# Kernel optimization log

Measured on AMD Instinct MI355X. Metric: run time of the kernel, lower is better.

The kernel has to match this reference:

```python
import jax, jax.numpy as jnp
import numpy as np

B, N, D, H, FF, L = 4, 256, 240, 8, 1024, 4
HD = D // H  # 30, divisible by 3 for 3D rotary
EPS = 1e-5


def setup_inputs() -> dict:
    key = jax.random.key(0)
    ks = iter(jax.random.split(key, 40))
    def nrm(shape, scale=1.0):
        return jax.random.normal(next(ks), shape, jnp.float32) * scale
    inp = {}
    for n in ["hand_token_t", "head_token_t", "hand_token_m1", "head_token_m1"]:
        inp[n] = nrm((B, N, D))
    for n in ["coords_hand_t", "coords_head_t", "coords_hand_m1", "coords_head_m1"]:
        inp[n] = jax.random.uniform(next(ks), (B, N, 3), jnp.float32)
    for n in ["state_t", "state_m1", "hand_pose_m1", "head_pose_m1", "hand_pose_t", "head_pose_t"]:
        inp[n] = nrm((B, D))
    sd = float(np.sqrt(2.0 / D))   # kaiming_normal fan_in=D
    sf = float(np.sqrt(2.0 / FF))  # kaiming_normal fan_in=FF
    inp["Wq"] = nrm((L, D, D), sd); inp["Wk"] = nrm((L, D, D), sd)
    inp["Wv"] = nrm((L, D, D), sd); inp["Wo"] = nrm((L, D, D), sd)
    inp["W1"] = nrm((L, FF, D), sd); inp["W2"] = nrm((L, D, FF), sf)
    inp["bq"] = jnp.zeros((L, D)); inp["bk"] = jnp.zeros((L, D))
    inp["bv"] = jnp.zeros((L, D)); inp["bo"] = jnp.zeros((L, D))
    inp["b1"] = jnp.zeros((L, FF)); inp["b2"] = jnp.zeros((L, D))
    inp["g1"] = jnp.ones((L, D)); inp["be1"] = jnp.zeros((L, D))
    inp["g2"] = jnp.ones((L, D)); inp["be2"] = jnp.zeros((L, D))
    return inp


def rope3d(x, coords):
    # x: (B,H,S,HD); coords: (B,S,3). head_dim split into 3 axis blocks,
    # each block rotated (interleaved pairs) by RoPE with pos = coord along that axis.
    d = HD // 3
    inv = 1.0 / (10000.0 ** (jnp.arange(0, d, 2, dtype=jnp.float32) / d))  # (d//2,)
    outs = []
    for a in range(3):
        xa = x[..., a * d:(a + 1) * d]
        ang = coords[:, None, :, a, None] * inv  # (B,1,S,d//2)
        c, s = jnp.cos(ang), jnp.sin(ang)
        x1, x2 = xa[..., 0::2], xa[..., 1::2]
        outs.append(jnp.stack([x1 * c - x2 * s, x1 * s + x2 * c], -1).reshape(xa.shape))
    if HD % 3:
        outs.append(x[..., 3 * d:])
    return jnp.concatenate(outs, -1)


def layernorm(x, g, b):
    m = x.mean(-1, keepdims=True)
    v = jnp.mean((x - m) ** 2, -1, keepdims=True)
    return (x - m) * jax.lax.rsqrt(v + EPS) * g + b


def _forward(hand_token_t, head_token_t, hand_token_m1, head_token_m1,
             coords_hand_t, coords_head_t, coords_hand_m1, coords_head_m1,
             state_t, state_m1, hand_pose_m1, head_pose_m1, hand_pose_t, head_pose_t,
             Wq, bq, Wk, bk, Wv, bv, Wo, bo, W1, b1, W2, b2, g1, be1, g2, be2):
    z3 = jnp.zeros((B, 1, 3), jnp.float32)
    src = jnp.concatenate([
        state_m1[:, None], hand_pose_m1[:, None], head_pose_m1[:, None],
        hand_token_m1, head_token_m1,
        state_t[:, None], hand_pose_t[:, None], head_pose_t[:, None],
        hand_token_t, head_token_t], axis=1)            # (B, S, D)
    cs = jnp.concatenate([z3, z3, z3, coords_hand_m1, coords_head_m1,
                          z3, z3, z3, coords_hand_t, coords_head_t], axis=1)  # (B, S, 3)
    S = src.shape[1]
    past = 1 + 2 + 2 * N  # current-frame tokens hide the past-frame keys
    mask = jnp.zeros((S, S), bool).at[past:, :past].set(True)
    scale = 1.0 / float(np.sqrt(HD))
    for l in range(L):
        q = (src @ Wq[l].T + bq[l]).reshape(B, S, H, HD).transpose(0, 2, 1, 3)
        k = (src @ Wk[l].T + bk[l]).reshape(B, S, H, HD).transpose(0, 2, 1, 3)
        v = (src @ Wv[l].T + bv[l]).reshape(B, S, H, HD).transpose(0, 2, 1, 3)
        q = rope3d(q, cs)
        k = rope3d(k, cs)
        scores = jnp.einsum('bhqd,bhkd->bhqk', q, k) * scale
        scores = jnp.where(mask, -jnp.inf, scores)
        attn = jnp.einsum('bhqk,bhkd->bhqd', jax.nn.softmax(scores, axis=-1), v)
        attn = attn.transpose(0, 2, 1, 3).reshape(B, S, D)
        s2 = layernorm(src + attn @ Wo[l].T + bo[l], g1[l], be1[l])
        ff = jax.nn.gelu(s2 @ W1[l].T + b1[l], approximate=False) @ W2[l].T + b2[l]
        src = layernorm(s2 + ff, g2[l], be2[l])
    return src[:, past:, :]


def reference(hand_token_t, head_token_t, hand_token_m1, head_token_m1,
              coords_hand_t, coords_head_t, coords_hand_m1, coords_head_m1,
              state_t, state_m1, hand_pose_m1, head_pose_m1, hand_pose_t, head_pose_t,
              Wq, bq, Wk, bk, Wv, bv, Wo, bo, W1, b1, W2, b2, g1, be1, g2, be2):
    return _forward(hand_token_t, head_token_t, hand_token_m1, head_token_m1,
                    coords_hand_t, coords_head_t, coords_hand_m1, coords_head_m1,
                    state_t, state_m1, hand_pose_m1, head_pose_m1, hand_pose_t, head_pose_t,
                    Wq, bq, Wk, bk, Wv, bv, Wo, bo, W1, b1, W2, b2, g1, be1, g2, be2)
```

## Files before the change

kernel.cpp:

```cpp
#include <hip/hip_runtime.h>
#include <cmath>

constexpr int cB = 4, cN = 256, cD = 240, cH = 8, cFF = 1024, cL = 4;
constexpr int cHD = 30;
constexpr int cS2 = 515;
constexpr int cBS2 = cB * cS2;
constexpr int cKp = 256;
constexpr int cSP2 = 576;
constexpr float EPSF = 1e-5f;

typedef __bf16 bf16x8 __attribute__((ext_vector_type(8)));
typedef float f32x4 __attribute__((ext_vector_type(4)));

__device__ inline unsigned short f2bf(float f) {
    unsigned int u = __builtin_bit_cast(unsigned int, f);
    unsigned int r = (u + 0x7fffu + ((u >> 16) & 1u)) >> 16;
    return (unsigned short)r;
}

constexpr int R1 = 4 * cL * 65536;
constexpr int R2 = R1 + cL * 1024 * 256;
constexpr int R3 = R2 + cL * 256 * 1024;
constexpr int R4 = R3 + cBS2 * cD;
constexpr int R5 = R4 + cBS2 * 15;
constexpr size_t qkvN = (size_t)cB * cH * cSP2 * 32;
constexpr int nSpan32 = (int)(3 * qkvN / 2);
constexpr int R6 = R5 + nSpan32;
constexpr int R7 = R6 + cBS2 * 8;

__global__ __launch_bounds__(256) void setup_all(
    const float* __restrict__ Wq, const float* __restrict__ Wk,
    const float* __restrict__ Wv, const float* __restrict__ Wo,
    const float* __restrict__ W1, const float* __restrict__ W2,
    const float* __restrict__ hand_t, const float* __restrict__ head_t,
    const float* __restrict__ state_t,
    const float* __restrict__ hand_pose_t, const float* __restrict__ head_pose_t,
    const float* __restrict__ ch_t, const float* __restrict__ cd_t,
    unsigned short* __restrict__ wqkv, unsigned short* __restrict__ w1p,
    unsigned short* __restrict__ w2p,
    float* __restrict__ src, unsigned short* __restrict__ sbf,
    float2* __restrict__ trig,
    unsigned int* __restrict__ qkvspan,
    unsigned short* __restrict__ padA, unsigned short* __restrict__ padB,
    unsigned short* __restrict__ padC)
{
    int idx = blockIdx.x * 256 + threadIdx.x;
    if (idx < R1) {
        int which = idx >> 18;
        const float* W = (which == 0) ? Wq : (which == 1) ? Wk : (which == 2) ? Wv : Wo;
        int rem = idx & 262143;
        int m = rem >> 16;
        int rc = rem & 65535;
        int r = rc >> 8, c = rc & 255;
        float v = (r < 240 && c < 240) ? W[((size_t)m * 240 + r) * 240 + c] : 0.f;
        wqkv[idx] = f2bf(v);
    } else if (idx < R2) {
        int rem = idx - R1;
        int m = rem >> 18;
        int rc = rem & 262143;
        int r = rc >> 8, c = rc & 255;
        float v = (c < 240) ? W1[((size_t)m * 1024 + r) * 240 + c] : 0.f;
        w1p[rem] = f2bf(v);
    } else if (idx < R3) {
        int rem = idx - R2;
        int m = rem >> 18;
        int rc = rem & 262143;
        int r = rc >> 10, c = rc & 1023;
        float v = (r < 240) ? W2[((size_t)m * 240 + r) * 1024 + c] : 0.f;
        w2p[rem] = f2bf(v);
    } else if (idx < R4) {
        int rem = idx - R3;
        int d = rem % cD;
        int r = rem / cD;
        int b = r / cS2, s = r % cS2;
        const float* p; int off;
        if (s == 0)          { p = state_t;      off = b * cD + d; }
        else if (s == 1)     { p = hand_pose_t;  off = b * cD + d; }
        else if (s == 2)     { p = head_pose_t;  off = b * cD + d; }
        else if (s < 259)    { p = hand_t;       off = (b * cN + (s - 3)) * cD + d; }
        else                 { p = head_t;       off = (b * cN + (s - 259)) * cD + d; }
        float v = p[off];
        src[rem] = v;
        sbf[(size_t)r * cKp + d] = f2bf(v);
    } else if (idx < R5) {
        int rem = idx - R4;
        int r = rem / 15, pair = rem - r * 15;
        int b = r / cS2, s = r % cS2;
        int a = pair / 5, j = pair - a * 5;
        float coord = 0.f;
        if (s >= 3 && s < 259)       coord = ch_t[(b * cN + (s - 3)) * 3 + a];
        else if (s >= 259)           coord = cd_t[(b * cN + (s - 259)) * 3 + a];
        float inv = __expf(-1.8420680743952367f * (float)j);
        float sn, co;
        sincosf(coord * inv, &sn, &co);
        trig[rem] = make_float2(co, sn);
    } else if (idx < R6) {
        qkvspan[idx - R5] = 0u;
    } else if (idx < R7) {
        int rem = idx - R6;
        int r = rem >> 3, j = rem & 7;
        ((unsigned int*)(padA + (size_t)r * 256 + 240))[j] = 0u;
        ((unsigned int*)(padB + (size_t)r * 256 + 240))[j] = 0u;
        ((unsigned int*)(padC + (size_t)r * 256 + 240))[j] = 0u;
    }
}

#define GEMM_CORE64(A_PTR, W_PTR, M_, KA_, NK_)                                               \
    __shared__ unsigned short Al[64][72];                                                     \
    __shared__ unsigned short Bl[64][72];                                                     \
    const int tid = threadIdx.x;                                                              \
    const int lane = tid & 63;                                                                \
    const int w = tid >> 6;                                                                   \
    const int wm = w >> 1, wn = w & 1;                                                        \
    const int lrow = lane & 15, kq = lane >> 4;                                               \
    const int colBase = blockIdx.x * 64;                                                      \
    const int sRow = tid >> 2;                                                                \
    const int sC = (tid & 3) * 16;                                                            \
    const int ar0 = min(rowBase + sRow, M_ - 1);                                              \
    const int wr = colBase + sRow;                                                            \
    const unsigned short* a0p = A_PTR + (size_t)ar0 * KA_ + sC;                               \
    const unsigned short* wp  = W_PTR + (size_t)wr * KA_ + sC;                                \
    f32x4 acc[2][2] = {};                                                                     \
    int4 rA0a = *(const int4*)a0p, rA0b = *(const int4*)(a0p + 8);                            \
    int4 rBa  = *(const int4*)wp,  rBb  = *(const int4*)(wp + 8);                             \
    for (int ks = 0; ks < NK_; ++ks) {                                                        \
        __syncthreads();                                                                      \
        *(int4*)&Al[sRow][sC]     = rA0a;                                                     \
        *(int4*)&Al[sRow][sC + 8] = rA0b;                                                     \
        *(int4*)&Bl[sRow][sC]     = rBa;                                                      \
        *(int4*)&Bl[sRow][sC + 8] = rBb;                                                      \
        __syncthreads();                                                                      \
        if (ks + 1 < NK_) {                                                                   \
            int kk = (ks + 1) * 64;                                                           \
            rA0a = *(const int4*)(a0p + kk); rA0b = *(const int4*)(a0p + kk + 8);             \
            rBa  = *(const int4*)(wp + kk);  rBb  = *(const int4*)(wp + kk + 8);              \
        }                                                                                     \
        _Pragma("unroll")                                                                     \
        for (int sub = 0; sub < 2; ++sub) {                                                   \
            bf16x8 af[2], bfr[2];                                                             \
            _Pragma("unroll")                                                                 \
            for (int i = 0; i < 2; ++i)                                                       \
                af[i] = *(const bf16x8*)&Al[wm * 32 + i * 16 + lrow][sub * 32 + kq * 8];      \
            _Pragma("unroll")                                                                 \
            for (int j = 0; j < 2; ++j)                                                       \
                bfr[j] = *(const bf16x8*)&Bl[wn * 32 + j * 16 + lrow][sub * 32 + kq * 8];     \
            _Pragma("unroll")                                                                 \
            for (int i = 0; i < 2; ++i)                                                       \
                _Pragma("unroll")                                                             \
                for (int j = 0; j < 2; ++j)                                                   \
                    acc[i][j] = __builtin_amdgcn_mfma_f32_16x16x32_bf16(af[i], bfr[j], acc[i][j], 0, 0, 0); \
        }                                                                                     \
    }

__global__ __launch_bounds__(256) void gemm_qkv_rope(
    const unsigned short* __restrict__ A,
    const unsigned short* __restrict__ Wqp, const unsigned short* __restrict__ Wkp,
    const unsigned short* __restrict__ Wvp,
    const float* __restrict__ bq, const float* __restrict__ bk, const float* __restrict__ bv,
    const float2* __restrict__ trig,
    unsigned short* __restrict__ qbf, unsigned short* __restrict__ kbf,
    unsigned short* __restrict__ vtbf)
{
    const int z = blockIdx.z;
    const unsigned short* Wsel = (z == 0) ? Wqp : (z == 1) ? Wkp : Wvp;
    const float* bias = (z == 0) ? bq : (z == 1) ? bk : bv;
    const int rowBase = blockIdx.y * 64;
    GEMM_CORE64(A, Wsel, cBS2, cKp, 4)
    if (z == 2) {
#pragma unroll
        for (int i = 0; i < 2; ++i) {
#pragma unroll
            for (int j = 0; j < 2; ++j) {
                int col = colBase + wn * 32 + j * 16 + lrow;
                if (col >= cD) continue;
                float bcol = bias[col];
                int hh = col / cHD, hd = col % cHD;
                f32x4 vv = acc[i][j];
                int row0 = rowBase + wm * 32 + i * 16 + kq * 4;
                int b0 = row0 / cS2, s0 = row0 - b0 * cS2;
                if (row0 + 3 < cBS2 && s0 + 3 < cS2) {
                    unsigned int lo = (unsigned)f2bf(vv[0] + bcol) | ((unsigned)f2bf(vv[1] + bcol) << 16);
                    unsigned int hi = (unsigned)f2bf(vv[2] + bcol) | ((unsigned)f2bf(vv[3] + bcol) << 16);
                    size_t base = ((size_t)(b0 * cH + hh) * 32 + hd) * cSP2 + s0;
                    *(unsigned int*)&vtbf[base]     = lo;
                    *(unsigned int*)&vtbf[base + 2] = hi;
                } else {
#pragma unroll
                    for (int r = 0; r < 4; ++r) {
                        int row = row0 + r;
                        if (row >= cBS2) continue;
                        int bb = row / cS2, ss = row - bb * cS2;
                        vtbf[((size_t)(bb * cH + hh) * 32 + hd) * cSP2 + ss] = f2bf(vv[r] + bcol);
                    }
                }
            }
        }
    } else {
        unsigned short* dst = (z == 0) ? qbf : kbf;
#pragma unroll
        for (int i = 0; i < 2; ++i) {
#pragma unroll
            for (int j = 0; j < 2; ++j) {
                int col = colBase + wn * 32 + j * 16 + lrow;
                bool colok = col < cD;
                int cc = colok ? col : 0;
                float bcol = colok ? bias[cc] : 0.f;
                int hh = cc / cHD, hd = cc % cHD;
                int a3 = hd / 10, jj = (hd % 10) >> 1;
                int pair = a3 * 5 + jj;
                f32x4 vv = acc[i][j];
#pragma unroll
                for (int r = 0; r < 2 * 2; ++r) {
                    int row = rowBase + wm * 32 + i * 16 + kq * 4 + r;
                    bool rowok = row < cBS2;
                    int rowc = rowok ? row : 0;
                    float val = vv[r] + bcol;
                    float pval = __shfl_xor(val, 1);
                    float2 t = trig[rowc * 15 + pair];
                    float outv = (hd & 1) ? (pval * t.y + val * t.x) : (val * t.x - pval * t.y);
                    if (colok && rowok) {
                        int b = rowc / cS2, s = rowc - b * cS2;
                        dst[((size_t)(b * cH + hh) * cSP2 + s) * 32 + hd] = f2bf(outv);
                    }
                }
            }
        }
    }
}

__global__ __launch_bounds__(256) void attn_mfma(
    const unsigned short* __restrict__ qbf, const unsigned short* __restrict__ kbf,
    const unsigned short* __restrict__ vtbf, unsigned short* __restrict__ outb)
{
    __shared__ unsigned short Pl[4][16][72];
    __shared__ float Ol[4][16][33];
    __shared__ float Ml[4][16];
    __shared__ float Ll[4][16];
    const int tid = threadIdx.x, lane = tid & 63, w = tid >> 6;
    const int bh = blockIdx.y, b = bh >> 3, h = bh & 7;
    const int qbase = blockIdx.x * 16;
    const int lr = lane & 15, lg = lane >> 4;
    const float scl = 0.18257418583505536f;
    const f32x4 czero = {0.f, 0.f, 0.f, 0.f};
    bf16x8 qf = *(const bf16x8*)&qbf[((size_t)bh * cSP2 + qbase + lr) * 32 + lg * 8];
    float m[4], l[4];
    f32x4 o0 = czero, o1 = czero;
#pragma unroll
    for (int r = 0; r < 4; ++r) { m[r] = -3.0e38f; l[r] = 0.f; }
    const int ts = (w * 9) / 4;
    const int te = ((w + 1) * 9) / 4;
    for (int tt = ts; tt < te; ++tt) {
        const int kb = tt * 64;
        f32x4 c[4];
#pragma unroll
        for (int t = 0; t < 4; ++t) {
            bf16x8 kf = *(const bf16x8*)&kbf[((size_t)bh * cSP2 + kb + 16 * t + lr) * 32 + lg * 8];
            c[t] = __builtin_amdgcn_mfma_f32_16x16x32_bf16(qf, kf, czero, 0, 0, 0);
        }
#pragma unroll
        for (int t = 0; t < 4; ++t) {
            bool koob = (kb + 16 * t + lr) >= cS2;
#pragma unroll
            for (int r = 0; r < 4; ++r)
                c[t][r] = koob ? -3.0e38f : c[t][r] * scl;
        }
        float mx[4];
#pragma unroll
        for (int r = 0; r < 4; ++r)
            mx[r] = fmaxf(fmaxf(c[0][r], c[1][r]), fmaxf(c[2][r], c[3][r]));
#pragma unroll
        for (int off = 1; off < 16; off <<= 1)
#pragma unroll
            for (int r = 0; r < 4; ++r)
                mx[r] = fmaxf(mx[r], __shfl_xor(mx[r], off));
        float corr[4], me[4], ps[4];
#pragma unroll
        for (int r = 0; r < 4; ++r) {
            float mn = fmaxf(m[r], mx[r]);
            corr[r] = __expf(m[r] - mn);
            m[r] = mn;
            me[r] = fmaxf(mn, -1.0e30f);
            ps[r] = 0.f;
        }
#pragma unroll
        for (int t = 0; t < 4; ++t)
#pragma unroll
            for (int r = 0; r < 4; ++r) {
                float p = __expf(c[t][r] - me[r]);
                c[t][r] = p;
                ps[r] += p;
            }
#pragma unroll
        for (int off = 1; off < 16; off <<= 1)
#pragma unroll
            for (int r = 0; r < 4; ++r)
                ps[r] += __shfl_xor(ps[r], off);
#pragma unroll
        for (int r = 0; r < 4; ++r) {
            l[r] = l[r] * corr[r] + ps[r];
            o0[r] *= corr[r];
            o1[r] *= corr[r];
        }
#pragma unroll
        for (int t = 0; t < 4; ++t)
#pragma unroll
            for (int r = 0; r < 4; ++r)
                Pl[w][lg * 4 + r][16 * t + lr] = f2bf(c[t][r]);
#pragma unroll
        for (int c2 = 0; c2 < 2; ++c2) {
            bf16x8 pa  = *(const bf16x8*)&Pl[w][lr][c2 * 32 + lg * 8];
            bf16x8 bv0 = *(const bf16x8*)&vtbf[((size_t)bh * 32 + lr) * cSP2 + kb + c2 * 32 + lg * 8];
            bf16x8 bv1 = *(const bf16x8*)&vtbf[((size_t)bh * 32 + 16 + lr) * cSP2 + kb + c2 * 32 + lg * 8];
            o0 = __builtin_amdgcn_mfma_f32_16x16x32_bf16(pa, bv0, o0, 0, 0, 0);
            o1 = __builtin_amdgcn_mfma_f32_16x16x32_bf16(pa, bv1, o1, 0, 0, 0);
        }
    }
#pragma unroll
    for (int r = 0; r < 4; ++r) {
        int row = lg * 4 + r;
        if (lr == 0) { Ml[w][row] = m[r]; Ll[w][row] = l[r]; }
        Ol[w][row][lr]      = o0[r];
        Ol[w][row][16 + lr] = o1[r];
    }
    __syncthreads();
    if (w == 0) {
        const int col = lane & 31, half = lane >> 5;
#pragma unroll
        for (int rr = 0; rr < 8; ++rr) {
            int row = half * 8 + rr;
            float M = fmaxf(fmaxf(Ml[0][row], Ml[1][row]), fmaxf(Ml[2][row], Ml[3][row]));
            float Lt = 0.f, Ot = 0.f;
#pragma unroll
            for (int ww = 0; ww < 4; ++ww) {
                float cc = __expf(Ml[ww][row] - M);
                Lt += Ll[ww][row] * cc;
                Ot += Ol[ww][row][col] * cc;
            }
            int qq = qbase + row;
            if (qq < cS2 && col < cHD)
                outb[((size_t)(b * cS2 + qq)) * cKp + h * cHD + col] = f2bf(Ot / Lt);
        }
    }
}

__global__ __launch_bounds__(256) void gemm_res64(
    const unsigned short* __restrict__ A, const unsigned short* __restrict__ W,
    const float* __restrict__ bias, const float* __restrict__ Rs,
    float* __restrict__ outF)
{
    const int rowBase = blockIdx.y * 64;
    GEMM_CORE64(A, W, cBS2, cKp, 4)
#pragma unroll
    for (int i = 0; i < 2; ++i) {
#pragma unroll
        for (int j = 0; j < 2; ++j) {
            int col = colBase + wn * 32 + j * 16 + lrow;
            if (col >= cD) continue;
            float bcol = bias[col];
            f32x4 v = acc[i][j];
#pragma unroll
            for (int r = 0; r < 4; ++r) {
                int row = rowBase + wm * 32 + i * 16 + kq * 4 + r;
                if (row >= cBS2) continue;
                outF[(size_t)row * cD + col] = v[r] + bcol + Rs[(size_t)row * cD + col];
            }
        }
    }
}

__global__ __launch_bounds__(256) void gemm_ff1(
    const unsigned short* __restrict__ A, const unsigned short* __restrict__ W,
    const float* __restrict__ bias, unsigned short* __restrict__ outB)
{
    const int rowBase = blockIdx.y * 64;
    GEMM_CORE64(A, W, cBS2, cKp, 4)
#pragma unroll
    for (int i = 0; i < 2; ++i) {
#pragma unroll
        for (int j = 0; j < 2; ++j) {
            int col = colBase + wn * 32 + j * 16 + lrow;
            float bcol = bias[col];
            f32x4 v = acc[i][j];
#pragma unroll
            for (int r = 0; r < 4; ++r) {
                int row = rowBase + wm * 32 + i * 16 + kq * 4 + r;
                if (row >= cBS2) continue;
                float t = v[r] + bcol;
                float gl = 0.5f * t * (1.0f + erff(t * 0.70710678118654752f));
                outB[(size_t)row * 1024 + col] = f2bf(gl);
            }
        }
    }
}

__global__ __launch_bounds__(256) void gemm_ff2_part(
    const unsigned short* __restrict__ A, const unsigned short* __restrict__ W,
    float* __restrict__ p0, float* __restrict__ p1)
{
    const int z = blockIdx.z;
    const int rowBase = blockIdx.y * 64;
    const unsigned short* Ap = A + z * 512;
    const unsigned short* Wp = W + z * 512;
    float* pF = z ? p1 : p0;
    GEMM_CORE64(Ap, Wp, cBS2, cFF, 8)
#pragma unroll
    for (int i = 0; i < 2; ++i) {
#pragma unroll
        for (int j = 0; j < 2; ++j) {
            int col = colBase + wn * 32 + j * 16 + lrow;
            if (col >= cD) continue;
            f32x4 v = acc[i][j];
#pragma unroll
            for (int r = 0; r < 4; ++r) {
                int row = rowBase + wm * 32 + i * 16 + kq * 4 + r;
                if (row >= cBS2) continue;
                pF[(size_t)row * cD + col] = v[r];
            }
        }
    }
}

__device__ inline void ln_core(float4 v, const float* __restrict__ g,
                               const float* __restrict__ be, float* __restrict__ yr,
                               unsigned short* __restrict__ br, int lane, bool ok)
{
    float sum = v.x + v.y + v.z + v.w;
#pragma unroll
    for (int off = 1; off < 64; off <<= 1) sum += __shfl_xor(sum, off);
    float mean = sum * (1.0f / cD);
    float vs = 0.f;
    if (ok) {
        float dx = v.x - mean, dy = v.y - mean, dz = v.z - mean, dw = v.w - mean;
        vs = dx * dx + dy * dy + dz * dz + dw * dw;
    }
#pragma unroll
    for (int off = 1; off < 64; off <<= 1) vs += __shfl_xor(vs, off);
    float rstd = rsqrtf(vs * (1.0f / cD) + EPSF);
    if (ok) {
        float4 g4 = *(const float4*)(g + 4 * lane);
        float4 b4 = *(const float4*)(be + 4 * lane);
        float4 y;
        y.x = (v.x - mean) * rstd * g4.x + b4.x;
        y.y = (v.y - mean) * rstd * g4.y + b4.y;
        y.z = (v.z - mean) * rstd * g4.z + b4.z;
        y.w = (v.w - mean) * rstd * g4.w + b4.w;
        *(float4*)(yr + 4 * lane) = y;
        if (br) {
            uint2 pk;
            pk.x = (unsigned)f2bf(y.x) | ((unsigned)f2bf(y.y) << 16);
            pk.y = (unsigned)f2bf(y.z) | ((unsigned)f2bf(y.w) << 16);
            *(uint2*)(br + 4 * lane) = pk;
        }
    }
}

__global__ __launch_bounds__(256) void ln_kernel(
    const float* __restrict__ x, const float* __restrict__ g,
    const float* __restrict__ be, float* __restrict__ y, unsigned short* __restrict__ ybf)
{
    int row = blockIdx.x * 4 + (threadIdx.x >> 6);
    int lane = threadIdx.x & 63;
    if (row >= cBS2) return;
    bool ok = lane < 60;
    float4 v = make_float4(0.f, 0.f, 0.f, 0.f);
    if (ok) v = *(const float4*)(x + (size_t)row * cD + 4 * lane);
    ln_core(v, g, be, y + (size_t)row * cD, ybf + (size_t)row * cKp, lane, ok);
}

__global__ __launch_bounds__(256) void ln2_kernel(
    const float* __restrict__ s2, const float* __restrict__ p0, const float* __restrict__ p1,
    const float* __restrict__ b2, const float* __restrict__ g, const float* __restrict__ be,
    float* __restrict__ y, unsigned short* __restrict__ ybf)
{
    int row = blockIdx.x * 4 + (threadIdx.x >> 6);
    int lane = threadIdx.x & 63;
    if (row >= cBS2) return;
    bool ok = lane < 60;
    float4 v = make_float4(0.f, 0.f, 0.f, 0.f);
    if (ok) {
        float4 a  = *(const float4*)(s2 + (size_t)row * cD + 4 * lane);
        float4 q0 = *(const float4*)(p0 + (size_t)row * cD + 4 * lane);
        float4 q1 = *(const float4*)(p1 + (size_t)row * cD + 4 * lane);
        float4 bb = *(const float4*)(b2 + 4 * lane);
        v.x = a.x + q0.x + q1.x + bb.x;
        v.y = a.y + q0.y + q1.y + bb.y;
        v.z = a.z + q0.z + q1.z + bb.z;
        v.w = a.w + q0.w + q1.w + bb.w;
    }
    ln_core(v, g, be, y + (size_t)row * cD, ybf + (size_t)row * cKp, lane, ok);
}

__global__ __launch_bounds__(256) void ln2_final(
    const float* __restrict__ s2, const float* __restrict__ p0, const float* __restrict__ p1,
    const float* __restrict__ b2, const float* __restrict__ g, const float* __restrict__ be,
    float* __restrict__ out)
{
    int row = blockIdx.x * 4 + (threadIdx.x >> 6);
    int lane = threadIdx.x & 63;
    if (row >= cBS2) return;
    bool ok = lane < 60;
    float4 v = make_float4(0.f, 0.f, 0.f, 0.f);
    if (ok) {
        float4 a  = *(const float4*)(s2 + (size_t)row * cD + 4 * lane);
        float4 q0 = *(const float4*)(p0 + (size_t)row * cD + 4 * lane);
        float4 q1 = *(const float4*)(p1 + (size_t)row * cD + 4 * lane);
        float4 bb = *(const float4*)(b2 + 4 * lane);
        v.x = a.x + q0.x + q1.x + bb.x;
        v.y = a.y + q0.y + q1.y + bb.y;
        v.z = a.z + q0.z + q1.z + bb.z;
        v.w = a.w + q0.w + q1.w + bb.w;
    }
    ln_core(v, g, be, out + (size_t)row * cD, nullptr, lane, ok);
}

extern "C" void kernel_launch(void* const* d_in, const int* in_sizes, int n_in,
                              void* d_out, int out_size, void* d_ws, size_t ws_size,
                              hipStream_t stream) {
    (void)in_sizes; (void)n_in; (void)out_size; (void)ws_size;
    const float* hand_t       = (const float*)d_in[0];
    const float* head_t       = (const float*)d_in[1];
    const float* c_hand_t     = (const float*)d_in[4];
    const float* c_head_t     = (const float*)d_in[5];
    const float* state_t      = (const float*)d_in[8];
    const float* hand_pose_t  = (const float*)d_in[12];
    const float* head_pose_t  = (const float*)d_in[13];
    const float* Wq = (const float*)d_in[14];
    const float* Wk = (const float*)d_in[15];
    const float* Wv = (const float*)d_in[16];
    const float* Wo = (const float*)d_in[17];
    const float* W1 = (const float*)d_in[18];
    const float* W2 = (const float*)d_in[19];
    const float* bq = (const float*)d_in[20];
    const float* bk = (const float*)d_in[21];
    const float* bv = (const float*)d_in[22];
    const float* bo = (const float*)d_in[23];
    const float* b1 = (const float*)d_in[24];
    const float* b2 = (const float*)d_in[25];
    const float* g1 = (const float*)d_in[26];
    const float* be1 = (const float*)d_in[27];
    const float* g2 = (const float*)d_in[28];
    const float* be2 = (const float*)d_in[29];

    char* p = (char*)d_ws;
    auto alloc_f = [&](size_t n) { float* r = (float*)p; p += n * sizeof(float); return r; };
    auto alloc_h = [&](size_t n) { unsigned short* r = (unsigned short*)p; p += n * sizeof(unsigned short); return r; };
    float* srcb  = alloc_f((size_t)cBS2 * cD);
    float* s2b   = alloc_f((size_t)cBS2 * cD);
    float* resid = alloc_f((size_t)cBS2 * cD);
    float* part1 = alloc_f((size_t)cBS2 * cD);
    float* trigf = alloc_f((size_t)cBS2 * 15 * 2);
    unsigned short* src_bf  = alloc_h((size_t)cBS2 * cKp);
    unsigned short* s2_bf   = alloc_h((size_t)cBS2 * cKp);
    unsigned short* attn_bf = alloc_h((size_t)cBS2 * cKp);
    unsigned short* ff_bf   = alloc_h((size_t)cBS2 * cFF);
    unsigned short* qbf  = alloc_h(qkvN);
    unsigned short* kbf  = alloc_h(qkvN);
    unsigned short* vtbf = alloc_h(qkvN);
    unsigned short* wqkv = alloc_h((size_t)4 * cL * 65536);
    unsigned short* w1p  = alloc_h((size_t)cL * 1024 * 256);
    unsigned short* w2p  = alloc_h((size_t)cL * 256 * 1024);
    float2* trig = (float2*)trigf;

    setup_all<<<(R7 + 255) / 256, 256, 0, stream>>>(
        Wq, Wk, Wv, Wo, W1, W2,
        hand_t, head_t, state_t, hand_pose_t, head_pose_t,
        c_hand_t, c_head_t,
        wqkv, w1p, w2p, srcb, src_bf, trig,
        (unsigned int*)qbf, src_bf, s2_bf, attn_bf);

    const int mT = (cBS2 + 63) / 64;
    for (int l = 0; l < cL; ++l) {
        const unsigned short* wq_l = wqkv + (size_t)(0 * cL + l) * 65536;
        const unsigned short* wk_l = wqkv + (size_t)(1 * cL + l) * 65536;
        const unsigned short* wv_l = wqkv + (size_t)(2 * cL + l) * 65536;
        const unsigned short* wo_l = wqkv + (size_t)(3 * cL + l) * 65536;
        const unsigned short* w1_l = w1p + (size_t)l * 1024 * 256;
        const unsigned short* w2_l = w2p + (size_t)l * 256 * 1024;
        const float* bq_l = bq + (size_t)l * cD;
        const float* bk_l = bk + (size_t)l * cD;
        const float* bv_l = bv + (size_t)l * cD;
        const float* bo_l = bo + (size_t)l * cD;
        const float* b1_l = b1 + (size_t)l * cFF;
        const float* b2_l = b2 + (size_t)l * cD;
        const float* g1_l = g1 + (size_t)l * cD;
        const float* be1_l = be1 + (size_t)l * cD;
        const float* g2_l = g2 + (size_t)l * cD;
        const float* be2_l = be2 + (size_t)l * cD;

        gemm_qkv_rope<<<dim3(4, mT, 3), 256, 0, stream>>>(
            src_bf, wq_l, wk_l, wv_l, bq_l, bk_l, bv_l, trig, qbf, kbf, vtbf);
        attn_mfma<<<dim3((cS2 + 15) / 16, cB * cH), 256, 0, stream>>>(
            qbf, kbf, vtbf, attn_bf);
        gemm_res64<<<dim3(4, mT), 256, 0, stream>>>(
            attn_bf, wo_l, bo_l, srcb, resid);
        ln_kernel<<<(cBS2 + 3) / 4, 256, 0, stream>>>(resid, g1_l, be1_l, s2b, s2_bf);
        gemm_ff1<<<dim3(16, mT), 256, 0, stream>>>(s2_bf, w1_l, b1_l, ff_bf);
        gemm_ff2_part<<<dim3(4, mT, 2), 256, 0, stream>>>(ff_bf, w2_l, resid, part1);
        if (l < cL - 1) {
            ln2_kernel<<<(cBS2 + 3) / 4, 256, 0, stream>>>(
                s2b, resid, part1, b2_l, g2_l, be2_l, srcb, src_bf);
        } else {
            ln2_final<<<(cBS2 + 3) / 4, 256, 0, stream>>>(
                s2b, resid, part1, b2_l, g2_l, be2_l, (float*)d_out);
        }
    }
}
```

Baseline: 247.6 us.

## Fuse bias, residual and LayerNorm into full-row GEMM epilogues

Adds a templated gemm_rowln kernel in which each block computes a 64x240 full-row output tile with MFMA. Bias, residual add and LayerNorm run in the epilogue, writing the fp32 and bf16 outputs directly. It replaces the Wo GEMM plus LayerNorm pair and the split-K FF2 GEMM plus LN2 pair, so two launches per layer and the fp32 intermediate round-trips go away. The cost is a much smaller grid (one block per 64 rows, about 33 blocks) with no split-K for the K=1024 FF2 GEMM, which may leave most CUs idle. Variance now uses E[x^2]-mean^2, which is less numerically robust.

```diff
diff --git a/kernel.cpp b/kernel.cpp
--- a/kernel.cpp
+++ b/kernel.cpp
@@ -210,7 +210,7 @@
                 int pair = a3 * 5 + jj;
                 f32x4 vv = acc[i][j];
 #pragma unroll
-                for (int r = 0; r < 2 * 2; ++r) {
+                for (int r = 0; r < 4; ++r) {
                     int row = rowBase + wm * 32 + i * 16 + kq * 4 + r;
                     bool rowok = row < cBS2;
                     int rowc = rowok ? row : 0;
@@ -343,26 +343,95 @@
     }
 }
 
-__global__ __launch_bounds__(256) void gemm_res64(
+template<int KA, int NK>
+__global__ __launch_bounds__(256) void gemm_rowln(
     const unsigned short* __restrict__ A, const unsigned short* __restrict__ W,
-    const float* __restrict__ bias, const float* __restrict__ Rs,
-    float* __restrict__ outF)
+    const float* __restrict__ bias, const float* __restrict__ resf,
+    const float* __restrict__ g, const float* __restrict__ be,
+    float* __restrict__ outF, unsigned short* __restrict__ outB)
 {
-    const int rowBase = blockIdx.y * 64;
-    GEMM_CORE64(A, W, cBS2, cKp, 4)
-#pragma unroll
-    for (int i = 0; i < 2; ++i) {
-#pragma unroll
-        for (int j = 0; j < 2; ++j) {
-            int col = colBase + wn * 32 + j * 16 + lrow;
-            if (col >= cD) continue;
-            float bcol = bias[col];
-            f32x4 v = acc[i][j];
-#pragma unroll
-            for (int r = 0; r < 4; ++r) {
-                int row = rowBase + wm * 32 + i * 16 + kq * 4 + r;
-                if (row >= cBS2) continue;
-                outF[(size_t)row * cD + col] = v[r] + bcol + Rs[(size_t)row * cD + col];
+    __shared__ unsigned short Al[64][72];
+    __shared__ unsigned short Wl[240][72];
+    const int tid = threadIdx.x;
+    const int lane = tid & 63;
+    const int w = tid >> 6;
+    const int lrow = lane & 15, kq = lane >> 4;
+    const int rowBase = blockIdx.x * 64;
+    const int aRow = tid >> 2, aC = (tid & 3) * 16;
+    const unsigned short* ap = A + (size_t)min(rowBase + aRow, cBS2 - 1) * KA + aC;
+    const unsigned short* wp = W + (size_t)tid * KA;
+    f32x4 acc[15] = {};
+    int4 rA0 = *(const int4*)ap, rA1 = *(const int4*)(ap + 8);
+    int4 rW[8];
+    if (tid < 240) {
+#pragma unroll
+        for (int i = 0; i < 8; ++i) rW[i] = *(const int4*)(wp + i * 8);
+    }
+    for (int ks = 0; ks < NK; ++ks) {
+        __syncthreads();
+        *(int4*)&Al[aRow][aC]     = rA0;
+        *(int4*)&Al[aRow][aC + 8] = rA1;
+        if (tid < 240) {
+#pragma unroll
+            for (int i = 0; i < 8; ++i) *(int4*)&Wl[tid][i * 8] = rW[i];
+        }
+        __syncthreads();
+        if (ks + 1 < NK) {
+            int kk = (ks + 1) * 64;
+            rA0 = *(const int4*)(ap + kk); rA1 = *(const int4*)(ap + kk + 8);
+            if (tid < 240) {
+#pragma unroll
+                for (int i = 0; i < 8; ++i) rW[i] = *(const int4*)(wp + kk + i * 8);
+            }
+        }
+#pragma unroll
+        for (int sub = 0; sub < 2; ++sub) {
+            bf16x8 av = *(const bf16x8*)&Al[w * 16 + lrow][sub * 32 + kq * 8];
+#pragma unroll
+            for (int f = 0; f < 15; ++f) {
+                bf16x8 wf = *(const bf16x8*)&Wl[f * 16 + lrow][sub * 32 + kq * 8];
+                acc[f] = __builtin_amdgcn_mfma_f32_16x16x32_bf16(wf, av, acc[f], 0, 0, 0);
+            }
+        }
+    }
+    const int row = rowBase + w * 16 + lrow;
+    const bool rok = row < cBS2;
+    const int rowc = min(row, cBS2 - 1);
+    float s1 = 0.f, sq = 0.f;
+#pragma unroll
+    for (int f = 0; f < 15; ++f) {
+        int col = f * 16 + kq * 4;
+        float4 b4 = *(const float4*)(bias + col);
+        float4 r4 = *(const float4*)(resf + (size_t)rowc * 240 + col);
+        acc[f][0] += b4.x + r4.x;
+        acc[f][1] += b4.y + r4.y;
+        acc[f][2] += b4.z + r4.z;
+        acc[f][3] += b4.w + r4.w;
+        s1 += acc[f][0] + acc[f][1] + acc[f][2] + acc[f][3];
+        sq += acc[f][0] * acc[f][0] + acc[f][1] * acc[f][1]
+            + acc[f][2] * acc[f][2] + acc[f][3] * acc[f][3];
+    }
+    s1 += __shfl_xor(s1, 16); s1 += __shfl_xor(s1, 32);
+    sq += __shfl_xor(sq, 16); sq += __shfl_xor(sq, 32);
+    float mean = s1 * (1.0f / cD);
+    float rstd = rsqrtf(sq * (1.0f / cD) - mean * mean + EPSF);
+    if (rok) {
+#pragma unroll
+        for (int f = 0; f < 15; ++f) {
+            int col = f * 16 + kq * 4;
+            float4 g4 = *(const float4*)(g + col);
+            float4 e4 = *(const float4*)(be + col);
+            float4 y;
+            y.x = (acc[f][0] - mean) * rstd * g4.x + e4.x;
+            y.y = (acc[f][1] - mean) * rstd * g4.y + e4.y;
+            y.z = (acc[f][2] - mean) * rstd * g4.z + e4.z;
+            y.w = (acc[f][3] - mean) * rstd * g4.w + e4.w;
+            *(float4*)(outF + (size_t)row * 240 + col) = y;
+            if (outB) {
+                uint2 pk;
+                pk.x = (unsigned)f2bf(y.x) | ((unsigned)f2bf(y.y) << 16);
+                pk.y = (unsigned)f2bf(y.z) | ((unsigned)f2bf(y.w) << 16);
+                *(uint2*)(outB + (size_t)row * cKp + col) = pk;
             }
         }
     }
@@ -391,126 +460,6 @@
             }
         }
     }
-}
-
-__global__ __launch_bounds__(256) void gemm_ff2_part(
-    const unsigned short* __restrict__ A, const unsigned short* __restrict__ W,
-    float* __restrict__ p0, float* __restrict__ p1)
-{
-    const int z = blockIdx.z;
-    const int rowBase = blockIdx.y * 64;
-    const unsigned short* Ap = A + z * 512;
-    const unsigned short* Wp = W + z * 512;
-    float* pF = z ? p1 : p0;
-    GEMM_CORE64(Ap, Wp, cBS2, cFF, 8)
-#pragma unroll
-    for (int i = 0; i < 2; ++i) {
-#pragma unroll
-        for (int j = 0; j < 2; ++j) {
-            int col = colBase + wn * 32 + j * 16 + lrow;
-            if (col >= cD) continue;
-            f32x4 v = acc[i][j];
-#pragma unroll
-            for (int r = 0; r < 4; ++r) {
-                int row = rowBase + wm * 32 + i * 16 + kq * 4 + r;
-                if (row >= cBS2) continue;
-                pF[(size_t)row * cD + col] = v[r];
-            }
-        }
-    }
-}
-
-__device__ inline void ln_core(float4 v, const float* __restrict__ g,
-                               const float* __restrict__ be, float* __restrict__ yr,
-                               unsigned short* __restrict__ br, int lane, bool ok)
-{
-    float sum = v.x + v.y + v.z + v.w;
-#pragma unroll
-    for (int off = 1; off < 64; off <<= 1) sum += __shfl_xor(sum, off);
-    float mean = sum * (1.0f / cD);
-    float vs = 0.f;
-    if (ok) {
-        float dx = v.x - mean, dy = v.y - mean, dz = v.z - mean, dw = v.w - mean;
-        vs = dx * dx + dy * dy + dz * dz + dw * dw;
-    }
-#pragma unroll
-    for (int off = 1; off < 64; off <<= 1) vs += __shfl_xor(vs, off);
-    float rstd = rsqrtf(vs * (1.0f / cD) + EPSF);
-    if (ok) {
-        float4 g4 = *(const float4*)(g + 4 * lane);
-        float4 b4 = *(const float4*)(be + 4 * lane);
-        float4 y;
-        y.x = (v.x - mean) * rstd * g4.x + b4.x;
-        y.y = (v.y - mean) * rstd * g4.y + b4.y;
-        y.z = (v.z - mean) * rstd * g4.z + b4.z;
-        y.w = (v.w - mean) * rstd * g4.w + b4.w;
-        *(float4*)(yr + 4 * lane) = y;
-        if (br) {
-            uint2 pk;
-            pk.x = (unsigned)f2bf(y.x) | ((unsigned)f2bf(y.y) << 16);
-            pk.y = (unsigned)f2bf(y.z) | ((unsigned)f2bf(y.w) << 16);
-            *(uint2*)(br + 4 * lane) = pk;
-        }
-    }
-}
-
-__global__ __launch_bounds__(256) void ln_kernel(
-    const float* __restrict__ x, const float* __restrict__ g,
-    const float* __restrict__ be, float* __restrict__ y, unsigned short* __restrict__ ybf)
-{
-    int row = blockIdx.x * 4 + (threadIdx.x >> 6);
-    int lane = threadIdx.x & 63;
-    if (row >= cBS2) return;
-    bool ok = lane < 60;
-    float4 v = make_float4(0.f, 0.f, 0.f, 0.f);
-    if (ok) v = *(const float4*)(x + (size_t)row * cD + 4 * lane);
-    ln_core(v, g, be, y + (size_t)row * cD, ybf + (size_t)row * cKp, lane, ok);
-}
-
-__global__ __launch_bounds__(256) void ln2_kernel(
-    const float* __restrict__ s2, const float* __restrict__ p0, const float* __restrict__ p1,
-    const float* __restrict__ b2, const float* __restrict__ g, const float* __restrict__ be,
-    float* __restrict__ y, unsigned short* __restrict__ ybf)
-{
-    int row = blockIdx.x * 4 + (threadIdx.x >> 6);
-    int lane = threadIdx.x & 63;
-    if (row >= cBS2) return;
-    bool ok = lane < 60;
-    float4 v = make_float4(0.f, 0.f, 0.f, 0.f);
-    if (ok) {
-        float4 a  = *(const float4*)(s2 + (size_t)row * cD + 4 * lane);
-        float4 q0 = *(const float4*)(p0 + (size_t)row * cD + 4 * lane);
-        float4 q1 = *(const float4*)(p1 + (size_t)row * cD + 4 * lane);
-        float4 bb = *(const float4*)(b2 + 4 * lane);
-        v.x = a.x + q0.x + q1.x + bb.x;
-        v.y = a.y + q0.y + q1.y + bb.y;
-        v.z = a.z + q0.z + q1.z + bb.z;
-        v.w = a.w + q0.w + q1.w + bb.w;
-    }
-    ln_core(v, g, be, y + (size_t)row * cD, ybf + (size_t)row * cKp, lane, ok);
-}
-
-__global__ __launch_bounds__(256) void ln2_final(
-    const float* __restrict__ s2, const float* __restrict__ p0, const float* __restrict__ p1,
-    const float* __restrict__ b2, const float* __restrict__ g, const float* __restrict__ be,
-    float* __restrict__ out)
-{
-    int row = blockIdx.x * 4 + (threadIdx.x >> 6);
-    int lane = threadIdx.x & 63;
-    if (row >= cBS2) return;
-    bool ok = lane < 60;
-    float4 v = make_float4(0.f, 0.f, 0.f, 0.f);
-    if (ok) {
-        float4 a  = *(const float4*)(s2 + (size_t)row * cD + 4 * lane);
-        float4 q0 = *(const float4*)(p0 + (size_t)row * cD + 4 * lane);
-        float4 q1 = *(const float4*)(p1 + (size_t)row * cD + 4 * lane);
-        float4 bb = *(const float4*)(b2 + 4 * lane);
-        v.x = a.x + q0.x + q1.x + bb.x;
-        v.y = a.y + q0.y + q1.y + bb.y;
-        v.z = a.z + q0.z + q1.z + bb.z;
-        v.w = a.w + q0.w + q1.w + bb.w;
-    }
-    ln_core(v, g, be, out + (size_t)row * cD, nullptr, lane, ok);
 }
 
 extern "C" void kernel_launch(void* const* d_in, const int* in_sizes, int n_in,
@@ -546,8 +495,6 @@
     auto alloc_h = [&](size_t n) { unsigned short* r = (unsigned short*)p; p += n * sizeof(unsigned short); return r; };
     float* srcb  = alloc_f((size_t)cBS2 * cD);
     float* s2b   = alloc_f((size_t)cBS2 * cD);
-    float* resid = alloc_f((size_t)cBS2 * cD);
-    float* part1 = alloc_f((size_t)cBS2 * cD);
     float* trigf = alloc_f((size_t)cBS2 * 15 * 2);
     unsigned short* src_bf  = alloc_h((size_t)cBS2 * cKp);
     unsigned short* s2_bf   = alloc_h((size_t)cBS2 * cKp);
@@ -591,17 +538,15 @@
             src_bf, wq_l, wk_l, wv_l, bq_l, bk_l, bv_l, trig, qbf, kbf, vtbf);
         attn_mfma<<<dim3((cS2 + 15) / 16, cB * cH), 256, 0, stream>>>(
             qbf, kbf, vtbf, attn_bf);
-        gemm_res64<<<dim3(4, mT), 256, 0, stream>>>(
-            attn_bf, wo_l, bo_l, srcb, resid);
-        ln_kernel<<<(cBS2 + 3) / 4, 256, 0, stream>>>(resid, g1_l, be1_l, s2b, s2_bf);
+        gemm_rowln<cKp, 4><<<mT, 256, 0, stream>>>(
+            attn_bf, wo_l, bo_l, srcb, g1_l, be1_l, s2b, s2_bf);
         gemm_ff1<<<dim3(16, mT), 256, 0, stream>>>(s2_bf, w1_l, b1_l, ff_bf);
-        gemm_ff2_part<<<dim3(4, mT, 2), 256, 0, stream>>>(ff_bf, w2_l, resid, part1);
         if (l < cL - 1) {
-            ln2_kernel<<<(cBS2 + 3) / 4, 256, 0, stream>>>(
-                s2b, resid, part1, b2_l, g2_l, be2_l, srcb, src_bf);
+            gemm_rowln<cFF, 16><<<mT, 256, 0, stream>>>(
+                ff_bf, w2_l, b2_l, s2b, g2_l, be2_l, srcb, src_bf);
         } else {
-            ln2_final<<<(cBS2 + 3) / 4, 256, 0, stream>>>(
-                s2b, resid, part1, b2_l, g2_l, be2_l, (float*)d_out);
-        }
-    }
-}
+            gemm_rowln<cFF, 16><<<mT, 256, 0, stream>>>(
+                ff_bf, w2_l, b2_l, s2b, g2_l, be2_l, (float*)d_out, nullptr);
+        }
+    }
+}
```

After: 514.5 us. +107.8%, slower.
